# Kernel tuning notes

Hardware: AMD Instinct MI355X
Metric: run time of the kernel (lower is better)

## Reference

```python
import jax, jax.numpy as jnp
import numpy as np

N = 100000      # nodes
E = 1600000     # edges (before self-loops)
IN_DIM = 128
HEADS = 4
C = 32          # hid_dim // heads = 128 // 4
SLOPE = 0.2     # PyG GATConv default negative_slope


def setup_inputs() -> dict:
    key = jax.random.key(0)
    k1, k2, k3, k4, k5 = jax.random.split(key, 5)
    x = jax.random.normal(k1, (N, IN_DIM), dtype=jnp.float32)
    edge_index = jax.random.randint(k2, (2, E), 0, N, dtype=jnp.int32)
    # learned parameters of GATConv
    W = jax.random.normal(k3, (IN_DIM, HEADS * C), dtype=jnp.float32) / np.sqrt(IN_DIM)
    att_src = jax.random.normal(k4, (HEADS, C), dtype=jnp.float32) * 0.1
    att_dst = jax.random.normal(k5, (HEADS, C), dtype=jnp.float32) * 0.1
    bias = jnp.zeros((HEADS * C,), dtype=jnp.float32)
    return {"x": x, "edge_index": edge_index, "W": W,
            "att_src": att_src, "att_dst": att_dst, "bias": bias}


def reference(x, edge_index, W, att_src, att_dst, bias):
    # PyG GATConv default add_self_loops=True
    loops = jnp.arange(N, dtype=edge_index.dtype)
    ei = jnp.concatenate([edge_index, jnp.stack([loops, loops])], axis=1)
    src, dst = ei[0], ei[1]                       # messages flow src -> dst

    h = (x @ W).reshape(N, HEADS, C)              # [N,H,C]
    a_src = jnp.einsum('nhc,hc->nh', h, att_src)  # [N,H]
    a_dst = jnp.einsum('nhc,hc->nh', h, att_dst)  # [N,H]

    e = a_src[src] + a_dst[dst]                   # [E+N,H] per-edge logits
    e = jax.nn.leaky_relu(e, SLOPE)

    # segment softmax over edges sharing a destination node
    m = jax.ops.segment_max(e, dst, num_segments=N)        # [N,H]
    e = jnp.exp(e - m[dst])
    s = jax.ops.segment_sum(e, dst, num_segments=N)        # [N,H]
    alpha = e / (s[dst] + 1e-16)                            # [E+N,H]

    msg = h[src] * alpha[:, :, None]                        # [E+N,H,C]
    out = jax.ops.segment_sum(msg, dst, num_segments=N)     # [N,H,C]
    return out.reshape(N, HEADS * C) + bias                 # concat heads + bias
```

## Files before the change

kernel.cpp:

```cpp
#include <hip/hip_runtime.h>
#include <cstddef>

#define HEADS 4
#define HC 128
#define SLOPE 0.2f
#define NPBUCK 256
#define NSBMAX 512
#define SBCAP 5120
#define CHUNK 4096

using half8 = __attribute__((ext_vector_type(8))) _Float16;
using f32x4 = __attribute__((ext_vector_type(4))) float;

__device__ __forceinline__ float edge_w(float v) {
    v = v > 0.f ? v : SLOPE * v;
    return __expf(v);
}
__device__ __forceinline__ float2 up2(unsigned w) {
    union { unsigned u; _Float16 f[2]; } c; c.u = w;
    return make_float2((float)c.f[0], (float)c.f[1]);
}

__global__ void wt_kernel(const float* __restrict__ W, _Float16* __restrict__ WTh) {
    int k = threadIdx.x;
    int nn = blockIdx.x;
    WTh[nn * HC + k] = (_Float16)W[k * HC + nn];
}

__global__ __launch_bounds__(256)
void gemm_att_count_kernel(const float* __restrict__ x, const _Float16* __restrict__ WTh,
                           const float* __restrict__ att_src, const float* __restrict__ att_dst,
                           _Float16* __restrict__ h2,
                           float* __restrict__ a_s, float* __restrict__ a_d,
                           const int* __restrict__ ei, int* __restrict__ cnt2d,
                           int gb, int E, int n) {
    __shared__ int cnt[NSBMAX];
    int tid = threadIdx.x;

    if (blockIdx.x >= gb) {
        int cb = blockIdx.x - gb;
        for (int i = tid; i < NSBMAX; i += 256) cnt[i] = 0;
        __syncthreads();
        int Etot = E + n;
        int e0 = cb * CHUNK;
        int eend = e0 + CHUNK; if (eend > Etot) eend = Etot;
        for (int e = e0 + tid; e < eend; e += 256) {
            int dst = (e < E) ? ei[E + e] : (e - E);
            atomicAdd(&cnt[dst >> 8], 1);
        }
        __syncthreads();
        int* row = cnt2d + (size_t)cb * NSBMAX;
        for (int i = tid; i < NSBMAX; i += 256) row[i] = cnt[i];
        return;
    }

    int wv   = tid >> 6;
    int lane = tid & 63;
    int t    = lane & 15;
    int q    = lane >> 4;
    int r0   = blockIdx.x * 64 + wv * 16;

    f32x4 acc[8];
#pragma unroll
    for (int ct = 0; ct < 8; ++ct) acc[ct] = (f32x4){0.f, 0.f, 0.f, 0.f};

    int  arow = r0 + t;
    bool aval = arow < n;
    const float* xp = x + (size_t)(aval ? arow : 0) * HC;

    for (int kc = 0; kc < 4; ++kc) {
        int k0 = kc * 32 + q * 8;
        half8 a;
        float4 fa = *(const float4*)(xp + k0);
        float4 fb = *(const float4*)(xp + k0 + 4);
        if (!aval) { fa = make_float4(0.f,0.f,0.f,0.f); fb = fa; }
        a[0] = (_Float16)fa.x; a[1] = (_Float16)fa.y;
        a[2] = (_Float16)fa.z; a[3] = (_Float16)fa.w;
        a[4] = (_Float16)fb.x; a[5] = (_Float16)fb.y;
        a[6] = (_Float16)fb.z; a[7] = (_Float16)fb.w;
#pragma unroll
        for (int ct = 0; ct < 8; ++ct) {
            half8 b = *(const half8*)(WTh + (size_t)(ct * 16 + t) * HC + k0);
            acc[ct] = __builtin_amdgcn_mfma_f32_16x16x32_f16(a, b, acc[ct], 0, 0, 0);
        }
    }

#pragma unroll
    for (int reg = 0; reg < 4; ++reg) {
        int row = r0 + q * 4 + reg;
        if (row < n) {
#pragma unroll
            for (int ct = 0; ct < 8; ++ct)
                h2[(size_t)row * HC + ct * 16 + t] = (_Float16)acc[ct][reg];
        }
    }

    float asv[8], adv[8];
#pragma unroll
    for (int ct = 0; ct < 8; ++ct) {
        asv[ct] = att_src[ct * 16 + t];
        adv[ct] = att_dst[ct * 16 + t];
    }
#pragma unroll
    for (int reg = 0; reg < 4; ++reg) {
        int row = r0 + q * 4 + reg;
        float4 ps, pd;
        ps.x = acc[0][reg]*asv[0] + acc[1][reg]*asv[1];
        ps.y = acc[2][reg]*asv[2] + acc[3][reg]*asv[3];
        ps.z = acc[4][reg]*asv[4] + acc[5][reg]*asv[5];
        ps.w = acc[6][reg]*asv[6] + acc[7][reg]*asv[7];
        pd.x = acc[0][reg]*adv[0] + acc[1][reg]*adv[1];
        pd.y = acc[2][reg]*adv[2] + acc[3][reg]*adv[3];
        pd.z = acc[4][reg]*adv[4] + acc[5][reg]*adv[5];
        pd.w = acc[6][reg]*adv[6] + acc[7][reg]*adv[7];
#pragma unroll
        for (int m = 1; m < 16; m <<= 1) {
            ps.x += __shfl_xor(ps.x, m); ps.y += __shfl_xor(ps.y, m);
            ps.z += __shfl_xor(ps.z, m); ps.w += __shfl_xor(ps.w, m);
            pd.x += __shfl_xor(pd.x, m); pd.y += __shfl_xor(pd.y, m);
            pd.z += __shfl_xor(pd.z, m); pd.w += __shfl_xor(pd.w, m);
        }
        if (t == 0 && row < n) {
            ((float4*)a_s)[row] = ps;
            ((float4*)a_d)[row] = pd;
        }
    }
}

__global__ __launch_bounds__(512)
void colscan_kernel(const int* __restrict__ cnt2d, int* __restrict__ base2d,
                    int* __restrict__ bucketend, int nchunks) {
    __shared__ int tmp[512];
    int b = blockIdx.x;
    int t = threadIdx.x;
    int v = (t < nchunks) ? cnt2d[(size_t)t * NSBMAX + b] : 0;
    tmp[t] = v;
    __syncthreads();
#pragma unroll
    for (int off = 1; off < 512; off <<= 1) {
        int u = (t >= off) ? tmp[t - off] : 0;
        __syncthreads();
        tmp[t] += u;
        __syncthreads();
    }
    if (t < nchunks) base2d[(size_t)t * NSBMAX + b] = b * SBCAP + tmp[t] - v;
    if (t == 511) bucketend[b] = b * SBCAP + tmp[511];
}

__global__ __launch_bounds__(256)
void scatter_kernel(const int* __restrict__ ei, int E, int n,
                    const int* __restrict__ base2d, int2* __restrict__ binned) {
    __shared__ int cur[NSBMAX];
    int tid = threadIdx.x;
    const int* row = base2d + (size_t)blockIdx.x * NSBMAX;
    for (int i = tid; i < NSBMAX; i += 256) cur[i] = row[i];
    __syncthreads();
    int Etot = E + n;
    int e0 = blockIdx.x * CHUNK;
    int eend = e0 + CHUNK; if (eend > Etot) eend = Etot;
    for (int e = e0 + tid; e < eend; e += 256) {
        int src, dst;
        if (e < E) { src = ei[e]; dst = ei[E + e]; }
        else       { src = e - E; dst = src; }
        int p = atomicAdd(&cur[dst >> 8], 1);
        binned[p] = make_int2(src, dst);
    }
}

__global__ __launch_bounds__(256)
void place_kernel(const int* __restrict__ bucketend, const int2* __restrict__ binned,
                  int* __restrict__ sorted, int* __restrict__ rowstart,
                  int* __restrict__ deg, int n) {
    __shared__ int cnt[256];
    __shared__ int pos[256];
    int b = blockIdx.x;
    int dst0 = b << 8;
    int rows = n - dst0; if (rows > 256) rows = 256;
    int tid = threadIdx.x;

    cnt[tid] = 0;
    __syncthreads();
    int wstart = b * SBCAP;
    int wend   = bucketend[b];
    for (int e = wstart + tid; e < wend; e += 256)
        atomicAdd(&cnt[binned[e].y - dst0], 1);
    __syncthreads();

    int d = cnt[tid];
    pos[tid] = d;
    __syncthreads();
#pragma unroll
    for (int off = 1; off < 256; off <<= 1) {
        int v = (tid >= off) ? pos[tid - off] : 0;
        __syncthreads();
        pos[tid] += v;
        __syncthreads();
    }
    int excl = pos[tid] - d;
    if (tid < rows) {
        rowstart[dst0 + tid] = wstart + excl;
        deg[dst0 + tid] = d;
    }
    cnt[tid] = excl;
    __syncthreads();
    for (int e = wstart + tid; e < wend; e += 256) {
        int2 ed = binned[e];
        int p = atomicAdd(&cnt[ed.y - dst0], 1);
        sorted[wstart + p] = ed.x;
    }
}

__global__ __launch_bounds__(256)
void agg_kernel(const int* __restrict__ rowstart, const int* __restrict__ deg,
                const int* __restrict__ sorted,
                const float* __restrict__ a_s, const float* __restrict__ a_d,
                const _Float16* __restrict__ h2, const float* __restrict__ bias,
                float* __restrict__ out, int n) {
    int dst = blockIdx.x * 4 + (threadIdx.x >> 6);
    if (dst >= n) return;
    int lane = threadIdx.x & 63;
    int li   = lane & 15;
    int sub  = lane >> 4;
    int head = li >> 2;
    int start = rowstart[dst];
    int cntv  = deg[dst];

    float ad = a_d[(size_t)dst * 4 + head];
    const uint4* h4 = (const uint4*)h2;
    float acc[8] = {0.f,0.f,0.f,0.f,0.f,0.f,0.f,0.f};
    float wsum = 0.f;

    for (int j = 0; j < cntv; j += 16) {
        int   sv[4]; float wv[4]; uint4 hv[4];
#pragma unroll
        for (int k = 0; k < 4; ++k) {
            int idx = j + k * 4 + sub;
            bool valid = idx < cntv;
            sv[k] = sorted[start + (valid ? idx : cntv - 1)];
            wv[k] = valid ? 1.f : 0.f;
        }
#pragma unroll
        for (int k = 0; k < 4; ++k)
            hv[k] = h4[(size_t)sv[k] * 16 + li];
#pragma unroll
        for (int k = 0; k < 4; ++k) {
            float w = wv[k] * edge_w(a_s[(size_t)sv[k] * 4 + head] + ad);
            float2 f0 = up2(hv[k].x), f1 = up2(hv[k].y),
                   f2 = up2(hv[k].z), f3 = up2(hv[k].w);
            acc[0] = fmaf(w, f0.x, acc[0]); acc[1] = fmaf(w, f0.y, acc[1]);
            acc[2] = fmaf(w, f1.x, acc[2]); acc[3] = fmaf(w, f1.y, acc[3]);
            acc[4] = fmaf(w, f2.x, acc[4]); acc[5] = fmaf(w, f2.y, acc[5]);
            acc[6] = fmaf(w, f3.x, acc[6]); acc[7] = fmaf(w, f3.y, acc[7]);
            wsum += w;
        }
    }

#pragma unroll
    for (int k = 0; k < 8; ++k) {
        acc[k] += __shfl_xor(acc[k], 16);
        acc[k] += __shfl_xor(acc[k], 32);
    }
    wsum += __shfl_xor(wsum, 16);
    wsum += __shfl_xor(wsum, 32);

    if (sub == 0) {
        float inv = 1.f / wsum;
        float4 b0 = ((const float4*)bias)[li * 2];
        float4 b1 = ((const float4*)bias)[li * 2 + 1];
        float4 o0 = make_float4(acc[0]*inv + b0.x, acc[1]*inv + b0.y,
                                acc[2]*inv + b0.z, acc[3]*inv + b0.w);
        float4 o1 = make_float4(acc[4]*inv + b1.x, acc[5]*inv + b1.y,
                                acc[6]*inv + b1.z, acc[7]*inv + b1.w);
        float4* op = (float4*)(out + (size_t)dst * HC);
        op[li * 2]     = o0;
        op[li * 2 + 1] = o1;
    }
}

extern "C" void kernel_launch(void* const* d_in, const int* in_sizes, int n_in,
                              void* d_out, int out_size, void* d_ws, size_t ws_size,
                              hipStream_t stream) {
    const float* x       = (const float*)d_in[0];
    const int*   ei      = (const int*)d_in[1];
    const float* W       = (const float*)d_in[2];
    const float* att_src = (const float*)d_in[3];
    const float* att_dst = (const float*)d_in[4];
    const float* bias    = (const float*)d_in[5];

    int n = in_sizes[0] / HC;
    int E = in_sizes[1] / 2;
    int Etot = E + n;
    int nbuck   = (n + NPBUCK - 1) / NPBUCK;
    int nchunks = (Etot + CHUNK - 1) / CHUNK;
    int gb      = (n + 63) / 64;

    _Float16* h2     = (_Float16*)d_ws;
    _Float16* WTh    = h2 + (size_t)n * HC;
    float* a_s       = (float*)(WTh + HC * HC);
    float* a_d       = a_s + (size_t)n * HEADS;
    int*   cnt2d     = (int*)(a_d + (size_t)n * HEADS);
    int*   base2d    = cnt2d + (size_t)nchunks * NSBMAX;
    int*   bucketend = base2d + (size_t)nchunks * NSBMAX;
    int*   rowstart  = bucketend + NSBMAX;
    int*   deg       = rowstart + n;
    int2*  binned    = (int2*)(deg + n);
    int*   sorted    = (int*)(binned + (size_t)nbuck * SBCAP);
    float* out       = (float*)d_out;

    wt_kernel<<<HC, HC, 0, stream>>>(W, WTh);
    gemm_att_count_kernel<<<gb + nchunks, 256, 0, stream>>>(
        x, WTh, att_src, att_dst, h2, a_s, a_d, ei, cnt2d, gb, E, n);
    colscan_kernel<<<nbuck, 512, 0, stream>>>(cnt2d, base2d, bucketend, nchunks);
    scatter_kernel<<<nchunks, 256, 0, stream>>>(ei, E, n, base2d, binned);
    place_kernel<<<nbuck, 256, 0, stream>>>(bucketend, binned, sorted,
                                            rowstart, deg, n);
    agg_kernel<<<(n + 3) / 4, 256, 0, stream>>>(rowstart, deg, sorted,
                                                a_s, a_d, h2, bias, out, n);
}
```

Baseline: 265.9 us.

## Stage GEMM tiles in LDS, drop colscan kernel, pack binned edges, halve agg group

The GEMM now stages the transposed weights and an fp16 x tile in shared memory, then writes h2 through LDS as coalesced 16-byte stores. The separate column-scan kernel is removed: each scatter block sums the earlier chunks' counts itself, which saves a launch but adds serial loads that grow with chunk index. Binned edges are packed into one int (src<<8 | local dst), halving that buffer's traffic. The aggregation kernel uses 32 threads per destination node instead of 64, so each block covers 8 nodes. This suits the low average degree but leaves fewer lanes to hide gather latency.

```diff
diff --git a/kernel.cpp b/kernel.cpp
--- a/kernel.cpp
+++ b/kernel.cpp
@@ -34,10 +34,11 @@
                            float* __restrict__ a_s, float* __restrict__ a_d,
                            const int* __restrict__ ei, int* __restrict__ cnt2d,
                            int gb, int E, int n) {
-    __shared__ int cnt[NSBMAX];
+    __shared__ __align__(16) char smem[34816 + 17408];
     int tid = threadIdx.x;
 
     if (blockIdx.x >= gb) {
+        int* cnt = (int*)smem;
         int cb = blockIdx.x - gb;
         for (int i = tid; i < NSBMAX; i += 256) cnt[i] = 0;
         __syncthreads();
@@ -54,44 +55,55 @@
         return;
     }
 
+    _Float16* wl = (_Float16*)smem;
+    _Float16* xh = (_Float16*)(smem + 34816);
+    int row0 = blockIdx.x * 64;
+
+    const uint4* WT4 = (const uint4*)WTh;
+#pragma unroll
+    for (int i = 0; i < 8; ++i) {
+        int j = tid + i * 256;
+        int r = j >> 4, c8 = j & 15;
+        *(uint4*)&wl[r * 136 + c8 * 8] = WT4[j];
+    }
+    const float4* x4 = (const float4*)x;
+#pragma unroll
+    for (int i = 0; i < 4; ++i) {
+        int j = tid + i * 256;
+        int r = j >> 4, c8 = j & 15;
+        int grow = row0 + r;
+        float4 fa = make_float4(0.f,0.f,0.f,0.f), fb = fa;
+        if (grow < n) {
+            fa = x4[(size_t)grow * 32 + c8 * 2];
+            fb = x4[(size_t)grow * 32 + c8 * 2 + 1];
+        }
+        half8 hv;
+        hv[0] = (_Float16)fa.x; hv[1] = (_Float16)fa.y;
+        hv[2] = (_Float16)fa.z; hv[3] = (_Float16)fa.w;
+        hv[4] = (_Float16)fb.x; hv[5] = (_Float16)fb.y;
+        hv[6] = (_Float16)fb.z; hv[7] = (_Float16)fb.w;
+        *(half8*)&xh[r * 136 + c8 * 8] = hv;
+    }
+    __syncthreads();
+
     int wv   = tid >> 6;
     int lane = tid & 63;
     int t    = lane & 15;
     int q    = lane >> 4;
-    int r0   = blockIdx.x * 64 + wv * 16;
+    int r0   = row0 + wv * 16;
 
     f32x4 acc[8];
 #pragma unroll
     for (int ct = 0; ct < 8; ++ct) acc[ct] = (f32x4){0.f, 0.f, 0.f, 0.f};
 
-    int  arow = r0 + t;
-    bool aval = arow < n;
-    const float* xp = x + (size_t)(aval ? arow : 0) * HC;
-
+#pragma unroll
     for (int kc = 0; kc < 4; ++kc) {
         int k0 = kc * 32 + q * 8;
-        half8 a;
-        float4 fa = *(const float4*)(xp + k0);
-        float4 fb = *(const float4*)(xp + k0 + 4);
-        if (!aval) { fa = make_float4(0.f,0.f,0.f,0.f); fb = fa; }
-        a[0] = (_Float16)fa.x; a[1] = (_Float16)fa.y;
-        a[2] = (_Float16)fa.z; a[3] = (_Float16)fa.w;
-        a[4] = (_Float16)fb.x; a[5] = (_Float16)fb.y;
-        a[6] = (_Float16)fb.z; a[7] = (_Float16)fb.w;
+        half8 a = *(const half8*)&xh[(wv * 16 + t) * 136 + k0];
 #pragma unroll
         for (int ct = 0; ct < 8; ++ct) {
-            half8 b = *(const half8*)(WTh + (size_t)(ct * 16 + t) * HC + k0);
+            half8 b = *(const half8*)&wl[(ct * 16 + t) * 136 + k0];
             acc[ct] = __builtin_amdgcn_mfma_f32_16x16x32_f16(a, b, acc[ct], 0, 0, 0);
-        }
-    }
-
-#pragma unroll
-    for (int reg = 0; reg < 4; ++reg) {
-        int row = r0 + q * 4 + reg;
-        if (row < n) {
-#pragma unroll
-            for (int ct = 0; ct < 8; ++ct)
-                h2[(size_t)row * HC + ct * 16 + t] = (_Float16)acc[ct][reg];
         }
     }
 
@@ -125,50 +137,54 @@
             ((float4*)a_d)[row] = pd;
         }
     }
-}
-
-__global__ __launch_bounds__(512)
-void colscan_kernel(const int* __restrict__ cnt2d, int* __restrict__ base2d,
-                    int* __restrict__ bucketend, int nchunks) {
-    __shared__ int tmp[512];
-    int b = blockIdx.x;
-    int t = threadIdx.x;
-    int v = (t < nchunks) ? cnt2d[(size_t)t * NSBMAX + b] : 0;
-    tmp[t] = v;
-    __syncthreads();
-#pragma unroll
-    for (int off = 1; off < 512; off <<= 1) {
-        int u = (t >= off) ? tmp[t - off] : 0;
-        __syncthreads();
-        tmp[t] += u;
-        __syncthreads();
-    }
-    if (t < nchunks) base2d[(size_t)t * NSBMAX + b] = b * SBCAP + tmp[t] - v;
-    if (t == 511) bucketend[b] = b * SBCAP + tmp[511];
+
+    __syncthreads();
+#pragma unroll
+    for (int reg = 0; reg < 4; ++reg)
+#pragma unroll
+        for (int ct = 0; ct < 8; ++ct)
+            xh[(wv * 16 + q * 4 + reg) * 136 + ct * 16 + t] = (_Float16)acc[ct][reg];
+    __syncthreads();
+#pragma unroll
+    for (int i = 0; i < 4; ++i) {
+        int j = tid + i * 256;
+        int r = j >> 4, c8 = j & 15;
+        int grow = row0 + r;
+        if (grow < n)
+            *(uint4*)&h2[(size_t)grow * HC + c8 * 8] = *(const uint4*)&xh[r * 136 + c8 * 8];
+    }
 }
 
 __global__ __launch_bounds__(256)
 void scatter_kernel(const int* __restrict__ ei, int E, int n,
-                    const int* __restrict__ base2d, int2* __restrict__ binned) {
+                    const int* __restrict__ cnt2d, int* __restrict__ bucketend,
+                    int* __restrict__ binned, int nchunks, int nbuck) {
     __shared__ int cur[NSBMAX];
     int tid = threadIdx.x;
-    const int* row = base2d + (size_t)blockIdx.x * NSBMAX;
-    for (int i = tid; i < NSBMAX; i += 256) cur[i] = row[i];
+    int c = blockIdx.x;
+    for (int b = tid; b < nbuck; b += 256) {
+        int s = 0;
+        for (int cc = 0; cc < c; ++cc) s += cnt2d[(size_t)cc * NSBMAX + b];
+        int base = b * SBCAP + s;
+        cur[b] = base;
+        if (c == nchunks - 1)
+            bucketend[b] = base + cnt2d[(size_t)c * NSBMAX + b];
+    }
     __syncthreads();
     int Etot = E + n;
-    int e0 = blockIdx.x * CHUNK;
+    int e0 = c * CHUNK;
     int eend = e0 + CHUNK; if (eend > Etot) eend = Etot;
     for (int e = e0 + tid; e < eend; e += 256) {
         int src, dst;
         if (e < E) { src = ei[e]; dst = ei[E + e]; }
         else       { src = e - E; dst = src; }
         int p = atomicAdd(&cur[dst >> 8], 1);
-        binned[p] = make_int2(src, dst);
+        binned[p] = (src << 8) | (dst & 255);
     }
 }
 
 __global__ __launch_bounds__(256)
-void place_kernel(const int* __restrict__ bucketend, const int2* __restrict__ binned,
+void place_kernel(const int* __restrict__ bucketend, const int* __restrict__ binned,
                   int* __restrict__ sorted, int* __restrict__ rowstart,
                   int* __restrict__ deg, int n) {
     __shared__ int cnt[256];
@@ -183,7 +199,7 @@
     int wstart = b * SBCAP;
     int wend   = bucketend[b];
     for (int e = wstart + tid; e < wend; e += 256)
-        atomicAdd(&cnt[binned[e].y - dst0], 1);
+        atomicAdd(&cnt[binned[e] & 255], 1);
     __syncthreads();
 
     int d = cnt[tid];
@@ -204,9 +220,9 @@
     cnt[tid] = excl;
     __syncthreads();
     for (int e = wstart + tid; e < wend; e += 256) {
-        int2 ed = binned[e];
-        int p = atomicAdd(&cnt[ed.y - dst0], 1);
-        sorted[wstart + p] = ed.x;
+        int p = binned[e];
+        int q = atomicAdd(&cnt[p & 255], 1);
+        sorted[wstart + q] = ((unsigned)p) >> 8;
     }
 }
 
@@ -216,11 +232,12 @@
                 const float* __restrict__ a_s, const float* __restrict__ a_d,
                 const _Float16* __restrict__ h2, const float* __restrict__ bias,
                 float* __restrict__ out, int n) {
-    int dst = blockIdx.x * 4 + (threadIdx.x >> 6);
+    int tid = threadIdx.x;
+    int dst = blockIdx.x * 8 + (tid >> 5);
     if (dst >= n) return;
-    int lane = threadIdx.x & 63;
-    int li   = lane & 15;
-    int sub  = lane >> 4;
+    int l32  = tid & 31;
+    int li   = l32 & 15;
+    int sub  = l32 >> 4;
     int head = li >> 2;
     int start = rowstart[dst];
     int cntv  = deg[dst];
@@ -230,21 +247,21 @@
     float acc[8] = {0.f,0.f,0.f,0.f,0.f,0.f,0.f,0.f};
     float wsum = 0.f;
 
-    for (int j = 0; j < cntv; j += 16) {
-        int   sv[4]; float wv[4]; uint4 hv[4];
+    for (int j = 0; j < cntv; j += 8) {
+        int sv[4]; float msk[4]; uint4 hv[4];
 #pragma unroll
         for (int k = 0; k < 4; ++k) {
-            int idx = j + k * 4 + sub;
+            int idx = j + k * 2 + sub;
             bool valid = idx < cntv;
-            sv[k] = sorted[start + (valid ? idx : cntv - 1)];
-            wv[k] = valid ? 1.f : 0.f;
+            sv[k]  = sorted[start + (valid ? idx : cntv - 1)];
+            msk[k] = valid ? 1.f : 0.f;
         }
 #pragma unroll
         for (int k = 0; k < 4; ++k)
             hv[k] = h4[(size_t)sv[k] * 16 + li];
 #pragma unroll
         for (int k = 0; k < 4; ++k) {
-            float w = wv[k] * edge_w(a_s[(size_t)sv[k] * 4 + head] + ad);
+            float w = msk[k] * edge_w(a_s[(size_t)sv[k] * 4 + head] + ad);
             float2 f0 = up2(hv[k].x), f1 = up2(hv[k].y),
                    f2 = up2(hv[k].z), f3 = up2(hv[k].w);
             acc[0] = fmaf(w, f0.x, acc[0]); acc[1] = fmaf(w, f0.y, acc[1]);
@@ -256,12 +273,8 @@
     }
 
 #pragma unroll
-    for (int k = 0; k < 8; ++k) {
-        acc[k] += __shfl_xor(acc[k], 16);
-        acc[k] += __shfl_xor(acc[k], 32);
-    }
+    for (int k = 0; k < 8; ++k) acc[k] += __shfl_xor(acc[k], 16);
     wsum += __shfl_xor(wsum, 16);
-    wsum += __shfl_xor(wsum, 32);
 
     if (sub == 0) {
         float inv = 1.f / wsum;
@@ -299,21 +312,20 @@
     float* a_s       = (float*)(WTh + HC * HC);
     float* a_d       = a_s + (size_t)n * HEADS;
     int*   cnt2d     = (int*)(a_d + (size_t)n * HEADS);
-    int*   base2d    = cnt2d + (size_t)nchunks * NSBMAX;
-    int*   bucketend = base2d + (size_t)nchunks * NSBMAX;
+    int*   bucketend = cnt2d + (size_t)nchunks * NSBMAX;
     int*   rowstart  = bucketend + NSBMAX;
     int*   deg       = rowstart + n;
-    int2*  binned    = (int2*)(deg + n);
-    int*   sorted    = (int*)(binned + (size_t)nbuck * SBCAP);
+    int*   binned    = deg + n;
+    int*   sorted    = binned + (size_t)nbuck * SBCAP;
     float* out       = (float*)d_out;
 
     wt_kernel<<<HC, HC, 0, stream>>>(W, WTh);
     gemm_att_count_kernel<<<gb + nchunks, 256, 0, stream>>>(
         x, WTh, att_src, att_dst, h2, a_s, a_d, ei, cnt2d, gb, E, n);
-    colscan_kernel<<<nbuck, 512, 0, stream>>>(cnt2d, base2d, bucketend, nchunks);
-    scatter_kernel<<<nchunks, 256, 0, stream>>>(ei, E, n, base2d, binned);
+    scatter_kernel<<<nchunks, 256, 0, stream>>>(ei, E, n, cnt2d, bucketend,
+                                                binned, nchunks, nbuck);
     place_kernel<<<nbuck, 256, 0, stream>>>(bucketend, binned, sorted,
                                             rowstart, deg, n);
-    agg_kernel<<<(n + 3) / 4, 256, 0, stream>>>(rowstart, deg, sorted,
+    agg_kernel<<<(n + 7) / 8, 256, 0, stream>>>(rowstart, deg, sorted,
                                                 a_s, a_d, h2, bias, out, n);
 }
```

Result: slower. 301.1 us (+13.2%).
